# Kernel optimization log

Measured on AMD Instinct MI355X. Metric: run time of the kernel, lower is better.

Reference implementation:

```python
import jax, jax.numpy as jnp
import numpy as np

LN_EPS = 1e-12


def setup_inputs() -> dict:
    key = jax.random.key(0)
    ks = jax.random.split(key, 10)
    B, S, W, D, H = 16, 512, 5, 200, 768
    std = 0.02
    return {
        "layer_output": jax.random.normal(ks[0], (B, S, H), dtype=jnp.float32),
        "word_embeddings": jax.random.normal(ks[1], (B, S, W, D), dtype=jnp.float32),
        "word_mask": jax.random.randint(ks[2], (B, S, W), 0, 2, dtype=jnp.int64),
        "W1": jax.random.normal(ks[3], (D, H), dtype=jnp.float32) * std,
        "b1": jnp.zeros((H,), dtype=jnp.float32),
        "W2": jax.random.normal(ks[4], (H, H), dtype=jnp.float32) * std,
        "b2": jnp.zeros((H,), dtype=jnp.float32),
        "attn_W": jax.random.normal(ks[5], (H, H), dtype=jnp.float32) * std,
        "ln_gamma": jnp.ones((H,), dtype=jnp.float32),
        "ln_beta": jnp.zeros((H,), dtype=jnp.float32),
    }


def reference(layer_output, word_embeddings, word_mask, W1, b1, W2, b2, attn_W, ln_gamma, ln_beta):
    # word_transform: Linear -> Tanh -> Linear (dropout = identity in eval)
    we = jnp.tanh(jnp.einsum("bswd,dh->bswh", word_embeddings, W1) + b1)
    we = jnp.einsum("bswh,hk->bswk", we, W2) + b2  # [B,S,W,H]

    # bilinear word attention: (x @ attn_W) . word_outputs -> score over W
    q = jnp.einsum("bsh,hk->bsk", layer_output, attn_W)  # [B,S,H]
    alpha = jnp.einsum("bsk,bswk->bsw", q, we)            # [B,S,W]
    alpha = alpha + (1.0 - word_mask.astype(alpha.dtype)) * -10000.0
    alpha = jax.nn.softmax(alpha, axis=-1)

    # weighted sum over words + residual
    agg = jnp.einsum("bsw,bswh->bsh", alpha, we)
    h = layer_output + agg

    # LayerNorm (fuse_layer; dropout = identity in eval)
    mu = jnp.mean(h, axis=-1, keepdims=True)
    var = jnp.mean(jnp.square(h - mu), axis=-1, keepdims=True)
    return (h - mu) * jax.lax.rsqrt(var + LN_EPS) * ln_gamma + ln_beta
```

## Files before the change

kernel.cpp:

```cpp
#include <hip/hip_runtime.h>
#include <hip/hip_bf16.h>
#include <math.h>


typedef __attribute__((ext_vector_type(8))) short bf16x8;
typedef __attribute__((ext_vector_type(4))) float f32x4;

__device__ __forceinline__ unsigned short f2bf_bits(float f) {
    __hip_bfloat16 h = __float2bfloat16(f);
    return *reinterpret_cast<unsigned short*>(&h);
}
__device__ __forceinline__ float bf_bits2f(unsigned short u) {
    union { unsigned int i; float f; } v; v.i = ((unsigned int)u) << 16; return v.f;
}
__device__ __forceinline__ float tanh_fast(float x) {
    float xc = fminf(fmaxf(x, -9.f), 9.f);
    float t  = __expf(2.f * xc);
    return (t - 1.f) * __builtin_amdgcn_rcpf(t + 1.f);
}

__device__ __forceinline__ void async_cp16(const void* g, void* lds) {
#if __has_builtin(__builtin_amdgcn_global_load_lds)
    auto gp = (const __attribute__((address_space(1))) unsigned int*)g;
    auto lp = (__attribute__((address_space(3))) unsigned int*)lds;
    __builtin_amdgcn_global_load_lds(gp, lp, 16, 0, 0);
#else
    *(uint4*)lds = *(const uint4*)g;
#endif
}

template<bool HAS_BIAS, bool TANH_ACT, bool RESID, bool OUT_BF16, int N, int K, int KREAL>
__device__ __forceinline__ void gemm_body(
    const __hip_bfloat16* __restrict__ A,
    const __hip_bfloat16* __restrict__ Bt,
    const float* __restrict__ bias,
    const float* __restrict__ resid,
    void* __restrict__ outp,
    int m0, int n0, unsigned char* smem)
{
    unsigned short* As = (unsigned short*)smem;
    unsigned short* Bs = (unsigned short*)(smem + 16384);

    const int tid  = threadIdx.x;
    const int lane = tid & 63;
    const int wave = tid >> 6;
    const int wm   = wave & 1;
    const int wn   = wave >> 1;

    const int rsub = lane >> 3;
    const int slot = lane & 7;
    const int kc   = slot ^ rsub;
    const __hip_bfloat16* gA = A  + (size_t)(m0 + wave * 32 + rsub) * K + kc * 8;
    const __hip_bfloat16* gB = Bt + (size_t)(n0 + wave * 32 + rsub) * K + kc * 8;
    unsigned short* lA = As + wave * 2048 + lane * 8;
    unsigned short* lB = Bs + wave * 2048 + lane * 8;

    const int row16 = lane & 15;
    const int kq    = lane >> 4;

    f32x4 acc[4][4];
#pragma unroll
    for (int i = 0; i < 4; i++)
#pragma unroll
        for (int j = 0; j < 4; j++) acc[i][j] = (f32x4){0.f, 0.f, 0.f, 0.f};

#pragma unroll
    for (int k0 = 0; k0 < K; k0 += 64) {
#pragma unroll
        for (int i = 0; i < 4; i++) {
            async_cp16(gA + (size_t)(8 * i) * K, lA + i * 512);
            async_cp16(gB + (size_t)(8 * i) * K, lB + i * 512);
        }
        gA += 64; gB += 64;
        __syncthreads();

        const bool full = (k0 + 32 < KREAL);

        bf16x8 af[2][4], bg[2][4];
#pragma unroll
        for (int mi = 0; mi < 4; mi++) {
            const int r = wm * 64 + mi * 16 + row16;
            af[0][mi] = *(const bf16x8*)&As[r * 64 + (kq ^ (r & 7)) * 8];
            if (full) af[1][mi] = *(const bf16x8*)&As[r * 64 + ((4 + kq) ^ (r & 7)) * 8];
        }
#pragma unroll
        for (int ni = 0; ni < 4; ni++) {
            const int r = wn * 64 + ni * 16 + row16;
            bg[0][ni] = *(const bf16x8*)&Bs[r * 64 + (kq ^ (r & 7)) * 8];
            if (full) bg[1][ni] = *(const bf16x8*)&Bs[r * 64 + ((4 + kq) ^ (r & 7)) * 8];
        }
#pragma unroll
        for (int mi = 0; mi < 4; mi++)
#pragma unroll
            for (int ni = 0; ni < 4; ni++)
                acc[mi][ni] = __builtin_amdgcn_mfma_f32_16x16x32_bf16(
                    af[0][mi], bg[0][ni], acc[mi][ni], 0, 0, 0);
        if (full) {
#pragma unroll
            for (int mi = 0; mi < 4; mi++)
#pragma unroll
                for (int ni = 0; ni < 4; ni++)
                    acc[mi][ni] = __builtin_amdgcn_mfma_f32_16x16x32_bf16(
                        af[1][mi], bg[1][ni], acc[mi][ni], 0, 0, 0);
        }
        __syncthreads();
    }

    if (OUT_BF16) {
        unsigned short* rep = (unsigned short*)smem;
#pragma unroll
        for (int ni = 0; ni < 4; ni++) {
            const int c = wn * 64 + ni * 16 + row16;
            float bcol = HAS_BIAS ? bias[n0 + c] : 0.f;
#pragma unroll
            for (int mi = 0; mi < 4; mi++)
#pragma unroll
                for (int r = 0; r < 4; r++) {
                    const int rr = wm * 64 + mi * 16 + kq * 4 + r;
                    float v = acc[mi][ni][r];
                    if (HAS_BIAS) v += bcol;
                    if (TANH_ACT) v = tanh_fast(v);
                    rep[rr * 128 + c] = f2bf_bits(v);
                }
        }
        __syncthreads();
#pragma unroll
        for (int p = 0; p < 8; p++) {
            const int lin = p * 256 + tid;
            const int row = lin >> 4;
            const int c8  = lin & 15;
            uint4 d = *(const uint4*)&rep[row * 128 + c8 * 8];
            *(uint4*)((__hip_bfloat16*)outp + (size_t)(m0 + row) * N + n0 + c8 * 8) = d;
        }
    } else {
        float* rep = (float*)smem;
#pragma unroll
        for (int h = 0; h < 2; h++) {
            if (wm == h) {
#pragma unroll
                for (int ni = 0; ni < 4; ni++) {
                    const int c = wn * 64 + ni * 16 + row16;
                    float bcol = HAS_BIAS ? bias[n0 + c] : 0.f;
#pragma unroll
                    for (int mi = 0; mi < 4; mi++)
#pragma unroll
                        for (int r = 0; r < 4; r++) {
                            const int rr = mi * 16 + kq * 4 + r;
                            float v = acc[mi][ni][r];
                            if (HAS_BIAS) v += bcol;
                            if (TANH_ACT) v = tanh_fast(v);
                            rep[rr * 128 + c] = v;
                        }
                }
            }
            __syncthreads();
#pragma unroll
            for (int p = 0; p < 8; p++) {
                const int lin = p * 256 + tid;
                const int row = lin >> 5;
                const int c4  = lin & 31;
                float4 v = *(const float4*)&rep[row * 128 + c4 * 4];
                const int grow = m0 + h * 64 + row;
                if (RESID) {
                    float4 rv = *(const float4*)&resid[(size_t)grow * N + n0 + c4 * 4];
                    v.x += rv.x; v.y += rv.y; v.z += rv.z; v.w += rv.w;
                }
                *(float4*)((float*)outp + (size_t)grow * N + n0 + c4 * 4) = v;
            }
            __syncthreads();
        }
    }
}

template<bool HAS_BIAS, bool TANH_ACT, bool RESID, bool OUT_BF16, int N, int K, int GX>
__global__ __launch_bounds__(256) void mfma_gemm(
    const __hip_bfloat16* __restrict__ A,
    const __hip_bfloat16* __restrict__ Bt,
    const float* __restrict__ bias,
    const float* __restrict__ resid,
    void* __restrict__ outp)
{
    __shared__ __align__(16) unsigned char smem[32768];
    int bx, by;
    {
        const int total = gridDim.x;
        const int per_xcd = total >> 3;
        if ((total & 7) == 0 && (per_xcd % GX) == 0) {
            int xcd = blockIdx.x & 7, idx = blockIdx.x >> 3;
            int lin = xcd * per_xcd + idx;
            by = lin / GX; bx = lin % GX;
        } else { by = blockIdx.x / GX; bx = blockIdx.x % GX; }
    }
    gemm_body<HAS_BIAS, TANH_ACT, RESID, OUT_BF16, N, K, K>(
        A, Bt, bias, resid, outp, by * 128, bx * 128, smem);
}

__global__ __launch_bounds__(256) void tct_kernel(
    const __hip_bfloat16* __restrict__ Eb,   const __hip_bfloat16* __restrict__ W1Tb,
    const float* __restrict__ b1,            __hip_bfloat16* __restrict__ Tb,
    const __hip_bfloat16* __restrict__ W2b,  const __hip_bfloat16* __restrict__ attnb,
    __hip_bfloat16* __restrict__ Ctb)
{
    __shared__ __align__(16) unsigned char smem[32768];
    if (blockIdx.x < 1920) {
        const int xcd = blockIdx.x & 7, idx = blockIdx.x >> 3;
        const int lin = xcd * 240 + idx;
        gemm_body<true, true, false, true, 768, 256, 224>(
            Eb, W1Tb, b1, nullptr, Tb, (lin / 6) * 128, (lin % 6) * 128, smem);
    } else {
        const int id = blockIdx.x - 1920;
        gemm_body<false, false, false, true, 768, 768, 768>(
            W2b, attnb, nullptr, nullptr, Ctb, (id / 6) * 128, (id % 6) * 128, smem);
    }
}

__global__ __launch_bounds__(256) void prep_kernel(
    const float* __restrict__ x,  __hip_bfloat16* __restrict__ xb,
    const float* __restrict__ w2, __hip_bfloat16* __restrict__ w2b,
    const float* __restrict__ aw, __hip_bfloat16* __restrict__ awb,
    const float* __restrict__ E,  __hip_bfloat16* __restrict__ Eb,
    const float* __restrict__ W1, __hip_bfloat16* __restrict__ W1Tb,
    __hip_bfloat16* __restrict__ W2Tb)
{
    __shared__ float tile[32][33];
    const int b = blockIdx.x, tid = threadIdx.x;
    if (b < 6144 + 576 + 576) {
        const float* src; __hip_bfloat16* dst; long long i;
        if (b < 6144)      { src = x;  dst = xb;  i = (long long)b * 256 + tid; }
        else if (b < 6720) { src = w2; dst = w2b; i = (long long)(b - 6144) * 256 + tid; }
        else               { src = aw; dst = awb; i = (long long)(b - 6720) * 256 + tid; }
        float4 v = ((const float4*)src)[i];
        ((ushort4*)dst)[i] = make_ushort4(f2bf_bits(v.x), f2bf_bits(v.y), f2bf_bits(v.z), f2bf_bits(v.w));
    } else if (b < 7296 + 10240) {
        const int lane = tid & 63, wave = tid >> 6;
        const long long row = (long long)(b - 7296) * 4 + wave;
        const int k = lane * 4;
        float4 v = make_float4(0.f, 0.f, 0.f, 0.f);
        if (k < 200) v = *(const float4*)&E[row * 200 + k];
        *(ushort4*)&Eb[row * 256 + k] =
            make_ushort4(f2bf_bits(v.x), f2bf_bits(v.y), f2bf_bits(v.z), f2bf_bits(v.w));
    } else {
        const float* in; __hip_bfloat16* outb; int R, C, Rpad, t;
        if (b < 17536 + 192) { t = b - 17536; in = W1; outb = W1Tb; R = 200; C = 768; Rpad = 256; }
        else                 { t = b - 17728; in = w2; outb = W2Tb; R = 768; C = 768; Rpad = 768; }
        const int c0 = (t % 24) * 32, r0 = (t / 24) * 32;
        const int xx = tid & 31, yy = tid >> 5;
#pragma unroll
        for (int i = 0; i < 32; i += 8) {
            int r = r0 + yy + i;
            tile[yy + i][xx] = (r < R) ? in[(size_t)r * C + c0 + xx] : 0.f;
        }
        __syncthreads();
#pragma unroll
        for (int i = 0; i < 32; i += 8)
            outb[(size_t)(c0 + yy + i) * Rpad + r0 + xx] = __float2bfloat16(tile[xx][yy + i]);
    }
}

__global__ __launch_bounds__(256) void attn_kernel(
    const __hip_bfloat16* __restrict__ T,
    const __hip_bfloat16* P,
    const int* __restrict__ mask,
    __hip_bfloat16* S)
{
    const int lane = threadIdx.x & 63;
    const int wave = threadIdx.x >> 6;
    const int r    = blockIdx.x * 4 + wave;
    const int base = lane * 12;

    float pv[12];
    {
        const ushort4* pp = (const ushort4*)((const unsigned short*)P + (size_t)r * 768 + base);
        ushort4 u0 = pp[0], u1 = pp[1], u2 = pp[2];
        unsigned short us[12] = {u0.x,u0.y,u0.z,u0.w, u1.x,u1.y,u1.z,u1.w, u2.x,u2.y,u2.z,u2.w};
#pragma unroll
        for (int j = 0; j < 12; j++) pv[j] = bf_bits2f(us[j]);
    }
    float tv[5][12], part[5];
#pragma unroll
    for (int w = 0; w < 5; w++) {
        const ushort4* tp = (const ushort4*)((const unsigned short*)T + ((size_t)r * 5 + w) * 768 + base);
        ushort4 u0 = tp[0], u1 = tp[1], u2 = tp[2];
        unsigned short us[12] = {u0.x,u0.y,u0.z,u0.w, u1.x,u1.y,u1.z,u1.w, u2.x,u2.y,u2.z,u2.w};
        float s = 0.f;
#pragma unroll
        for (int j = 0; j < 12; j++) { tv[w][j] = bf_bits2f(us[j]); s += tv[w][j] * pv[j]; }
        part[w] = s;
    }
#pragma unroll
    for (int off = 32; off > 0; off >>= 1)
#pragma unroll
        for (int w = 0; w < 5; w++)
            part[w] += __shfl_xor(part[w], off, 64);

    float logit[5], mx = -1e30f;
#pragma unroll
    for (int w = 0; w < 5; w++) {
        float m = (float)mask[(size_t)r * 5 + w];
        logit[w] = part[w] - 10000.0f * (1.0f - m);
        mx = fmaxf(mx, logit[w]);
    }
    float se = 0.f;
#pragma unroll
    for (int w = 0; w < 5; w++) { logit[w] = expf(logit[w] - mx); se += logit[w]; }
    const float inv = 1.0f / se;

    unsigned short os[12];
#pragma unroll
    for (int j = 0; j < 12; j++) {
        float s = 0.f;
#pragma unroll
        for (int w = 0; w < 5; w++) s += logit[w] * tv[w][j];
        os[j] = f2bf_bits(s * inv);
    }
    ushort4* sp = (ushort4*)((unsigned short*)S + (size_t)r * 768 + base);
    sp[0] = make_ushort4(os[0], os[1], os[2],  os[3]);
    sp[1] = make_ushort4(os[4], os[5], os[6],  os[7]);
    sp[2] = make_ushort4(os[8], os[9], os[10], os[11]);
}

__global__ __launch_bounds__(256) void ln_kernel(
    const float* __restrict__ Hbuf, const float* __restrict__ gamma,
    const float* __restrict__ beta, float* __restrict__ out)
{
    const int lane = threadIdx.x & 63;
    const int wave = threadIdx.x >> 6;
    const int r    = blockIdx.x * 4 + wave;
    const float* hr = Hbuf + (size_t)r * 768 + lane * 12;

    float v[12];
    {
        float4 a = *(const float4*)(hr);
        float4 b = *(const float4*)(hr + 4);
        float4 c = *(const float4*)(hr + 8);
        v[0]=a.x; v[1]=a.y; v[2]=a.z; v[3]=a.w;
        v[4]=b.x; v[5]=b.y; v[6]=b.z; v[7]=b.w;
        v[8]=c.x; v[9]=c.y; v[10]=c.z; v[11]=c.w;
    }
    float s = 0.f;
#pragma unroll
    for (int j = 0; j < 12; j++) s += v[j];
#pragma unroll
    for (int off = 32; off > 0; off >>= 1) s += __shfl_xor(s, off, 64);
    const float mu = s * (1.f / 768.f);
    float vs = 0.f;
#pragma unroll
    for (int j = 0; j < 12; j++) { float d = v[j] - mu; vs += d * d; }
#pragma unroll
    for (int off = 32; off > 0; off >>= 1) vs += __shfl_xor(vs, off, 64);
    const float rs = rsqrtf(vs * (1.f / 768.f) + 1e-12f);

    float o[12];
#pragma unroll
    for (int j = 0; j < 12; j++) {
        int h = lane * 12 + j;
        o[j] = (v[j] - mu) * rs * gamma[h] + beta[h];
    }
    float* orow = out + (size_t)r * 768 + lane * 12;
    *(float4*)(orow)     = make_float4(o[0], o[1], o[2],  o[3]);
    *(float4*)(orow + 4) = make_float4(o[4], o[5], o[6],  o[7]);
    *(float4*)(orow + 8) = make_float4(o[8], o[9], o[10], o[11]);
}

extern "C" void kernel_launch(void* const* d_in, const int* in_sizes, int n_in,
                              void* d_out, int out_size, void* d_ws, size_t ws_size,
                              hipStream_t stream)
{
    const float* x      = (const float*)d_in[0];
    const float* E      = (const float*)d_in[1];
    const int*   mask   = (const int*)d_in[2];
    const float* W1     = (const float*)d_in[3];
    const float* b1     = (const float*)d_in[4];
    const float* W2     = (const float*)d_in[5];
    const float* b2     = (const float*)d_in[6];
    const float* attn_W = (const float*)d_in[7];
    const float* gamma  = (const float*)d_in[8];
    const float* beta   = (const float*)d_in[9];
    float* out = (float*)d_out;

    const int BS = 8192, H = 768, M1 = 40960, KP = 256;

    char* p = (char*)d_ws;
    auto alloc = [&](size_t bytes) { char* q = p; p += (bytes + 255) & ~(size_t)255; return q; };
    __hip_bfloat16* xb    = (__hip_bfloat16*)alloc((size_t)BS * H * 2);
    __hip_bfloat16* W2b   = (__hip_bfloat16*)alloc((size_t)H * H * 2);
    __hip_bfloat16* W2Tb  = (__hip_bfloat16*)alloc((size_t)H * H * 2);
    __hip_bfloat16* attnb = (__hip_bfloat16*)alloc((size_t)H * H * 2);
    __hip_bfloat16* Ctb   = (__hip_bfloat16*)alloc((size_t)H * H * 2);
    __hip_bfloat16* W1Tb  = (__hip_bfloat16*)alloc((size_t)H * KP * 2);
    __hip_bfloat16* Tb    = (__hip_bfloat16*)alloc((size_t)M1 * H * 2);
    __hip_bfloat16* Eb    = (__hip_bfloat16*)alloc((size_t)M1 * KP * 2);
    float* Hb = (float*)Tb;
    __hip_bfloat16* Pb = Eb;
    __hip_bfloat16* Sb = Pb;

    prep_kernel<<<18304, 256, 0, stream>>>(x, xb, W2, W2b, attn_W, attnb,
                                           E, Eb, W1, W1Tb, W2Tb);

    tct_kernel<<<1956, 256, 0, stream>>>(Eb, W1Tb, b1, Tb, W2b, attnb, Ctb);

    mfma_gemm<false, false, false, true, 768, 768, 6><<<384, 256, 0, stream>>>(
        xb, Ctb, nullptr, nullptr, Pb);
    attn_kernel<<<BS / 4, 256, 0, stream>>>(Tb, Pb, mask, Sb);
    mfma_gemm<true, false, true, false, 768, 768, 6><<<384, 256, 0, stream>>>(
        Sb, W2Tb, b2, x, Hb);
    ln_kernel<<<BS / 4, 256, 0, stream>>>(Hb, gamma, beta, out);
}
```

Before: 217.6 us.

## Double-buffer GEMM LDS tiles with async prefetch and pad epilogue staging

The GEMM main loop now uses two LDS buffers and prefetches k-tile t+2 while computing tile t. Explicit vmcnt waits and raw barriers replace __syncthreads, so loads overlap the MFMA work. The epilogue staging stride is padded from 128 to 132 to cut LDS bank conflicts, and the long K=768 blocks are moved to the front of the grid so they start first. LDS use doubles to 64KB per block, which can lower occupancy.

```diff
diff --git a/kernel.cpp b/kernel.cpp
--- a/kernel.cpp
+++ b/kernel.cpp
@@ -29,6 +29,11 @@
 #endif
 }
 
+__device__ __forceinline__ void sched_fence()  { asm volatile("" ::: "memory"); }
+__device__ __forceinline__ void wait8_barrier(){ asm volatile("s_waitcnt vmcnt(8)\ns_barrier" ::: "memory"); }
+__device__ __forceinline__ void wait0_barrier(){ asm volatile("s_waitcnt vmcnt(0)\ns_barrier" ::: "memory"); }
+__device__ __forceinline__ void barrier_only() { asm volatile("s_barrier" ::: "memory"); }
+
 template<bool HAS_BIAS, bool TANH_ACT, bool RESID, bool OUT_BF16, int N, int K, int KREAL>
 __device__ __forceinline__ void gemm_body(
     const __hip_bfloat16* __restrict__ A,
@@ -38,8 +43,7 @@
     void* __restrict__ outp,
     int m0, int n0, unsigned char* smem)
 {
-    unsigned short* As = (unsigned short*)smem;
-    unsigned short* Bs = (unsigned short*)(smem + 16384);
+    constexpr int NIT = K / 64;
 
     const int tid  = threadIdx.x;
     const int lane = tid & 63;
@@ -52,8 +56,8 @@
     const int kc   = slot ^ rsub;
     const __hip_bfloat16* gA = A  + (size_t)(m0 + wave * 32 + rsub) * K + kc * 8;
     const __hip_bfloat16* gB = Bt + (size_t)(n0 + wave * 32 + rsub) * K + kc * 8;
-    unsigned short* lA = As + wave * 2048 + lane * 8;
-    unsigned short* lB = Bs + wave * 2048 + lane * 8;
+    unsigned short* lA0 = (unsigned short*)smem + wave * 2048 + lane * 8;
+    unsigned short* lB0 = lA0 + 8192;
 
     const int row16 = lane & 15;
     const int kq    = lane >> 4;
@@ -64,17 +68,29 @@
 #pragma unroll
         for (int j = 0; j < 4; j++) acc[i][j] = (f32x4){0.f, 0.f, 0.f, 0.f};
 
-#pragma unroll
-    for (int k0 = 0; k0 < K; k0 += 64) {
+    auto stage = [&](int t) {
+        unsigned short* lA = lA0 + (t & 1) * 16384;
+        unsigned short* lB = lB0 + (t & 1) * 16384;
+        const __hip_bfloat16* a = gA + t * 64;
+        const __hip_bfloat16* b = gB + t * 64;
 #pragma unroll
         for (int i = 0; i < 4; i++) {
-            async_cp16(gA + (size_t)(8 * i) * K, lA + i * 512);
-            async_cp16(gB + (size_t)(8 * i) * K, lB + i * 512);
-        }
-        gA += 64; gB += 64;
-        __syncthreads();
-
-        const bool full = (k0 + 32 < KREAL);
+            async_cp16(a + (size_t)(8 * i) * K, lA + i * 512);
+            async_cp16(b + (size_t)(8 * i) * K, lB + i * 512);
+        }
+        sched_fence();
+    };
+
+    stage(0);
+    if (NIT > 1) stage(1);
+
+#pragma unroll
+    for (int t = 0; t < NIT; ++t) {
+        if (t == NIT - 1) wait0_barrier(); else wait8_barrier();
+
+        const unsigned short* As = (const unsigned short*)(smem + (t & 1) * 32768);
+        const unsigned short* Bs = As + 8192;
+        const bool full = (t * 64 + 32 < KREAL);
 
         bf16x8 af[2][4], bg[2][4];
 #pragma unroll
@@ -103,7 +119,8 @@
                     acc[mi][ni] = __builtin_amdgcn_mfma_f32_16x16x32_bf16(
                         af[1][mi], bg[1][ni], acc[mi][ni], 0, 0, 0);
         }
-        __syncthreads();
+        barrier_only();
+        if (t + 2 < NIT) stage(t + 2);
     }
 
     if (OUT_BF16) {
@@ -120,7 +137,7 @@
                     float v = acc[mi][ni][r];
                     if (HAS_BIAS) v += bcol;
                     if (TANH_ACT) v = tanh_fast(v);
-                    rep[rr * 128 + c] = f2bf_bits(v);
+                    rep[rr * 132 + c] = f2bf_bits(v);
                 }
         }
         __syncthreads();
@@ -129,8 +146,11 @@
             const int lin = p * 256 + tid;
             const int row = lin >> 4;
             const int c8  = lin & 15;
-            uint4 d = *(const uint4*)&rep[row * 128 + c8 * 8];
-            *(uint4*)((__hip_bfloat16*)outp + (size_t)(m0 + row) * N + n0 + c8 * 8) = d;
+            const unsigned short* s = &rep[row * 132 + c8 * 8];
+            union { uint4 u; unsigned long long q[2]; } d;
+            d.q[0] = *(const unsigned long long*)(s);
+            d.q[1] = *(const unsigned long long*)(s + 4);
+            *(uint4*)((__hip_bfloat16*)outp + (size_t)(m0 + row) * N + n0 + c8 * 8) = d.u;
         }
     } else {
         float* rep = (float*)smem;
@@ -149,7 +169,7 @@
                             float v = acc[mi][ni][r];
                             if (HAS_BIAS) v += bcol;
                             if (TANH_ACT) v = tanh_fast(v);
-                            rep[rr * 128 + c] = v;
+                            rep[rr * 132 + c] = v;
                         }
                 }
             }
@@ -159,7 +179,7 @@
                 const int lin = p * 256 + tid;
                 const int row = lin >> 5;
                 const int c4  = lin & 31;
-                float4 v = *(const float4*)&rep[row * 128 + c4 * 4];
+                float4 v = *(const float4*)&rep[row * 132 + c4 * 4];
                 const int grow = m0 + h * 64 + row;
                 if (RESID) {
                     float4 rv = *(const float4*)&resid[(size_t)grow * N + n0 + c4 * 4];
@@ -180,7 +200,7 @@
     const float* __restrict__ resid,
     void* __restrict__ outp)
 {
-    __shared__ __align__(16) unsigned char smem[32768];
+    __shared__ __align__(16) unsigned char smem[65536];
     int bx, by;
     {
         const int total = gridDim.x;
@@ -201,16 +221,17 @@
     const __hip_bfloat16* __restrict__ W2b,  const __hip_bfloat16* __restrict__ attnb,
     __hip_bfloat16* __restrict__ Ctb)
 {
-    __shared__ __align__(16) unsigned char smem[32768];
-    if (blockIdx.x < 1920) {
-        const int xcd = blockIdx.x & 7, idx = blockIdx.x >> 3;
+    __shared__ __align__(16) unsigned char smem[65536];
+    if (blockIdx.x < 36) {
+        const int id = blockIdx.x;
+        gemm_body<false, false, false, true, 768, 768, 768>(
+            W2b, attnb, nullptr, nullptr, Ctb, (id / 6) * 128, (id % 6) * 128, smem);
+    } else {
+        const int idq = blockIdx.x - 36;
+        const int xcd = idq & 7, idx = idq >> 3;
         const int lin = xcd * 240 + idx;
         gemm_body<true, true, false, true, 768, 256, 224>(
             Eb, W1Tb, b1, nullptr, Tb, (lin / 6) * 128, (lin % 6) * 128, smem);
-    } else {
-        const int id = blockIdx.x - 1920;
-        gemm_body<false, false, false, true, 768, 768, 768>(
-            W2b, attnb, nullptr, nullptr, Ctb, (id / 6) * 128, (id % 6) * 128, smem);
     }
 }
 
```

Measured after the change: 211.8 us. 1.03x faster.
